# Performance work log

Measured on AMD Instinct MI355X. Metric: run time of the kernel, lower is better.

The kernel has to match this reference:

```python
import jax, jax.numpy as jnp
import numpy as np

B, LR_DIM, G_DIM, K, D, T = 256, 1024, 512, 64, 256, 8
GRID = jnp.linspace(-4.0, 4.0, 41)  # registered buffer in torch module


def _mu_bell(x, c, a_bell, b_bell):
    # generalized bell membership, clamp(a,b) >= 1e-3 as in torch
    a = jnp.maximum(a_bell, 1e-3)
    b = jnp.maximum(b_bell, 1e-3)
    return 1.0 / (1.0 + jnp.abs((x - c) / a) ** (2.0 * b))


def _mu_s(x, a, b):
    eps = 1e-12
    a2 = jnp.minimum(a, b)
    b2 = jnp.maximum(a, b)
    mid = (a2 + b2) * 0.5
    up = 2.0 * ((x - a2) / (b2 - a2 + eps)) ** 2
    dn = 1.0 - 2.0 * ((b2 - x) / (b2 - a2 + eps)) ** 2
    y = jnp.where((x > a2) & (x <= mid), up, jnp.zeros_like(x))
    y = jnp.where((x > mid) & (x <= b2), dn, y)
    return jnp.where(x > b2, jnp.ones_like(x), y)


def _fuzzify(x, a_bell, b_bell):
    # x: (B,d) -> (B,2d)
    xs = 4.0 * jnp.tanh(x / 4.0)
    xb = _mu_bell(xs, 0.0, a_bell, b_bell)
    xS = _mu_s(xs, -1.0, 1.0)
    return jnp.concatenate([xb, xS], axis=-1)


def _defuzzify(rt, a_bell, b_bell):
    # rt: (B,2d) -> centroid (B,d)
    d = rt.shape[1] // 2
    rb, rs = rt[:, :d], rt[:, d:]
    g = GRID[None, None, :]                      # (1,1,G)
    c_b = 4.0 * jnp.tanh(rb)[..., None]          # (B,d,1)
    c_s = 4.0 * jnp.tanh(rs)[..., None]
    mu_b = _mu_bell(g, c_b, a_bell, b_bell)      # (B,d,G)
    a_s = jnp.clip(c_s - 1.0, -4.0, 4.0)
    b_s = jnp.clip(c_s + 1.0, -4.0, 4.0)
    mu_s = _mu_s(g, a_s, b_s)
    cen_b = (g * mu_b).sum(-1) / (mu_b.sum(-1) + 1e-12)
    cen_s = (g * mu_s).sum(-1) / (mu_s.sum(-1) + 1e-12)
    return 0.5 * cen_b + 0.5 * cen_s


def _forward(wsi_lr, genomics, FT, W_lr, b_lr, W_g, b_g, WqI, WqG, WkI, WkG,
             WvI, WvG, mlp_W1, mlp_b1, mlp_W2, mlp_b2, Wf, bf, Wi, bi, Vf, Vi,
             a_bell, b_bell):
    scale = jnp.float32(D) ** 0.5
    lr = wsi_lr @ W_lr + b_lr                    # (B,d)
    g = genomics @ W_g + b_g
    lr_f = _fuzzify(lr, a_bell, b_bell)          # (B,2d)
    g_f = _fuzzify(g, a_bell, b_bell)
    QI = lr_f @ WqI                              # (B,d), loop-invariant
    QG = g_f @ WqG
    Ft0 = jnp.broadcast_to(FT[None], (wsi_lr.shape[0],) + FT.shape)  # (B,K,d)

    def step(Ft, _):
        sI = jnp.einsum('bd,bkd->bk', QI, Ft @ WkI) / scale
        sG = jnp.einsum('bd,bkd->bk', QG, Ft @ WkG) / scale
        rtI = jnp.einsum('bk,bke->be', jax.nn.softmax(sI, axis=-1), Ft @ WvI)  # (B,2d)
        rtG = jnp.einsum('bk,bke->be', jax.nn.softmax(sG, axis=-1), Ft @ WvG)
        r = 0.5 * _defuzzify(rtI, a_bell, b_bell) + 0.5 * _defuzzify(rtG, a_bell, b_bell)
        rb = jnp.broadcast_to(r[:, None, :], Ft.shape)              # (B,K,d)
        x = Ft + rb
        F_tilde = jax.nn.gelu(x @ mlp_W1 + mlp_b1, approximate=False) @ mlp_W2 + mlp_b2 + x
        f_gate = jax.nn.sigmoid(rb @ Wf + bf + jnp.tanh(Ft @ Vf))
        i_gate = jax.nn.sigmoid(rb @ Wi + bi + jnp.tanh(Ft @ Vi))
        Ft_new = f_gate * Ft + i_gate * jnp.tanh(F_tilde)
        return Ft_new, Ft_new

    _, steps = jax.lax.scan(step, Ft0, None, length=T)
    # torch stores step `T-s` result at index s-1: list index 0 holds the LAST
    # computed state, index T-1 the first -> reverse chronological order
    return steps[::-1]  # (T,B,K,d)


def setup_inputs() -> dict:
    key = jax.random.key(0)
    ks = jax.random.split(key, 20)

    def rn(k, shape, scale):
        return jax.random.normal(k, shape, dtype=jnp.float32) * scale

    z = lambda *s: jnp.zeros(s, jnp.float32)
    return dict(
        wsi_lr=rn(ks[0], (B, LR_DIM), 1.0),
        genomics=rn(ks[1], (B, G_DIM), 1.0),
        FT=rn(ks[2], (K, D), 0.02),
        W_lr=rn(ks[3], (LR_DIM, D), LR_DIM ** -0.5), b_lr=z(D),
        W_g=rn(ks[4], (G_DIM, D), G_DIM ** -0.5), b_g=z(D),
        WqI=rn(ks[5], (2 * D, D), (2 * D) ** -0.5),
        WqG=rn(ks[6], (2 * D, D), (2 * D) ** -0.5),
        WkI=rn(ks[7], (D, D), D ** -0.5),
        WkG=rn(ks[8], (D, D), D ** -0.5),
        WvI=rn(ks[9], (D, 2 * D), D ** -0.5),
        WvG=rn(ks[10], (D, 2 * D), D ** -0.5),
        mlp_W1=rn(ks[11], (D, 2 * D), D ** -0.5), mlp_b1=z(2 * D),
        mlp_W2=rn(ks[12], (2 * D, D), (2 * D) ** -0.5), mlp_b2=z(D),
        Wf=rn(ks[13], (D, D), D ** -0.5), bf=z(D),
        Wi=rn(ks[14], (D, D), D ** -0.5), bi=z(D),
        Vf=rn(ks[15], (D, D), D ** -0.5),
        Vi=rn(ks[16], (D, D), D ** -0.5),
        a_bell=jnp.float32(1.0),
        b_bell=jnp.float32(2.0),
    )


def reference(wsi_lr, genomics, FT, W_lr, b_lr, W_g, b_g, WqI, WqG, WkI, WkG,
              WvI, WvG, mlp_W1, mlp_b1, mlp_W2, mlp_b2, Wf, bf, Wi, bi, Vf, Vi,
              a_bell, b_bell):
    return _forward(wsi_lr, genomics, FT, W_lr, b_lr, W_g, b_g, WqI, WqG, WkI,
                    WkG, WvI, WvG, mlp_W1, mlp_b1, mlp_W2, mlp_b2, Wf, bf, Wi,
                    bi, Vf, Vi, a_bell, b_bell)
```

## Files before the change

kernel.cpp:

```cpp
#include <hip/hip_runtime.h>
#include <hip/hip_bf16.h>

#define B_    256
#define K_    64
#define D_    256
#define T_    8
#define NROW  (B_*K_)

typedef short short8v __attribute__((ext_vector_type(8)));
typedef float f32x4  __attribute__((ext_vector_type(4)));

__device__ __forceinline__ float fexp2(float x) { return __builtin_amdgcn_exp2f(x); }
__device__ __forceinline__ float flog2(float x) { return __builtin_amdgcn_logf(x); }

__device__ __forceinline__ float sigmoid_f(float x) {
  return 1.f / (1.f + fexp2(x * -1.4426950408889634f));
}
__device__ __forceinline__ float tanh_fast(float x) {
  float xc = fminf(fmaxf(x, -30.f), 30.f);
  float t = fexp2(xc * 2.8853900817779268f);
  return (t - 1.f) / (t + 1.f);
}
__device__ __forceinline__ float gelu_f(float x) {
  return 0.5f * x * (1.f + erff(x * 0.70710678118654752440f));
}
__device__ __forceinline__ unsigned short f2bf(float x) {
  __hip_bfloat16 h = __float2bfloat16(x);
  return *reinterpret_cast<unsigned short*>(&h);
}
__device__ __forceinline__ float bfss(unsigned short s) {
  return __uint_as_float(((unsigned int)s) << 16);
}
__device__ __forceinline__ float muS_f(float x, float a2, float b2) {
  float mid = 0.5f * (a2 + b2);
  float inv = 1.f / (b2 - a2 + 1e-12f);
  if (x > b2)  return 1.f;
  if (x > mid) { float u = (b2 - x) * inv; return 1.f - 2.f * u * u; }
  if (x > a2)  { float u = (x - a2) * inv; return 2.f * u * u; }
  return 0.f;
}
__device__ __forceinline__ float pow_abs(float z, float e2b) {
  return fexp2(e2b * flog2(fabsf(z)));
}
__device__ __forceinline__ float defuzz_one(float rb_, float rs_, float ab, float bb) {
  float e2b = 2.f * bb;
  float inv_ab = 1.f / ab;
  float cb = 4.f * tanh_fast(rb_);
  float num = 0.f, den = 0.f;
  #pragma unroll
  for (int j = 0; j < 41; ++j) {
    float gj = -4.f + 0.2f * (float)j;
    float mu = 1.f / (1.f + pow_abs((gj - cb) * inv_ab, e2b));
    num += gj * mu; den += mu;
  }
  float cenb = num / (den + 1e-12f);
  float cs = 4.f * tanh_fast(rs_);
  float as_ = fminf(fmaxf(cs - 1.f, -4.f), 4.f);
  float bs_ = fminf(fmaxf(cs + 1.f, -4.f), 4.f);
  num = 0.f; den = 0.f;
  {
    float mid = 0.5f * (as_ + bs_);
    float inv = 1.f / (bs_ - as_ + 1e-12f);
    #pragma unroll
    for (int j = 0; j < 41; ++j) {
      float gj = -4.f + 0.2f * (float)j;
      float mu;
      if (gj > bs_)      mu = 1.f;
      else if (gj > mid) { float u = (bs_ - gj) * inv; mu = 1.f - 2.f * u * u; }
      else if (gj > as_) { float u = (gj - as_) * inv; mu = 2.f * u * u; }
      else               mu = 0.f;
      num += gj * mu; den += mu;
    }
  }
  float cens = num / (den + 1e-12f);
  return 0.5f * cenb + 0.5f * cens;
}

__global__ __launch_bounds__(256) void k_convert(
    const float* __restrict__ W1, const float* __restrict__ Vf, const float* __restrict__ Vi,
    const float* __restrict__ W2, const float* __restrict__ FT,
    const float* __restrict__ WkI, const float* __restrict__ WkG,
    unsigned short* __restrict__ B1t, unsigned short* __restrict__ W2t,
    unsigned short* __restrict__ FTbf,
    float* __restrict__ WkIt, float* __restrict__ WkGt)
{
  int idx = blockIdx.x * 256 + threadIdx.x;
  if (idx < 262144) {
    int n = idx >> 8, k = idx & 255;
    float v = (n < 512) ? W1[(size_t)k*512 + n]
            : (n < 768) ? Vf[(size_t)k*256 + (n-512)]
                        : Vi[(size_t)k*256 + (n-768)];
    B1t[idx] = f2bf(v);
  } else if (idx < 393216) {
    int j = idx - 262144;
    int n = j >> 9, k = j & 511;
    W2t[j] = f2bf(W2[(size_t)k*256 + n]);
  } else if (idx < 409600) {
    int j = idx - 393216;
    FTbf[j] = f2bf(FT[j]);
  } else if (idx < 475136) {
    int j = idx - 409600;
    int k = j >> 8, n = j & 255;
    WkIt[j] = WkI[(size_t)n*256 + k];
  } else if (idx < 540672) {
    int j = idx - 475136;
    int k = j >> 8, n = j & 255;
    WkGt[j] = WkG[(size_t)n*256 + k];
  }
}

__global__ __launch_bounds__(256) void k_pre_lin(
    const float* __restrict__ wsi, const float* __restrict__ gen,
    const float* __restrict__ W_lr, const float* __restrict__ b_lr,
    const float* __restrict__ W_g,  const float* __restrict__ b_g,
    const float* __restrict__ a_p,  const float* __restrict__ b_p,
    float* __restrict__ lrf, float* __restrict__ gf)
{
  int g_ix = blockIdx.x;
  int half = g_ix >> 4, tile = g_ix & 15;
  int bx = tile & 3, by = tile >> 2;
  int n0 = bx * 64, m0 = by * 64;
  const float* A    = half ? gen  : wsi;
  const float* Bm   = half ? W_g  : W_lr;
  const float* bias = half ? b_g  : b_lr;
  float* outp       = half ? gf   : lrf;
  int KK            = half ? 512  : 1024;
  float ab = fmaxf(a_p[0], 0.001f), bb = fmaxf(b_p[0], 0.001f);
  float e2b = 2.f * bb, inv_ab = 1.f / ab;

  __shared__ float As[16][64];
  __shared__ float Bs[16][64];
  int tid = threadIdx.x, tx = tid & 15, ty = tid >> 4;
  float acc[4][4] = {};
  int am = tid >> 2, ak = (tid & 3) * 4;
  int bk = tid >> 4, bn = (tid & 15) * 4;
  const float* arow = A + (size_t)(m0 + am) * KK;
  for (int k0 = 0; k0 < KK; k0 += 16) {
    float4 av = *(const float4*)(arow + k0 + ak);
    As[ak+0][am] = av.x; As[ak+1][am] = av.y; As[ak+2][am] = av.z; As[ak+3][am] = av.w;
    *(float4*)&Bs[bk][bn] = *(const float4*)(Bm + (size_t)(k0 + bk) * 256 + n0 + bn);
    __syncthreads();
    #pragma unroll
    for (int kk = 0; kk < 16; ++kk) {
      float a0 = As[kk][ty*4+0], a1 = As[kk][ty*4+1], a2 = As[kk][ty*4+2], a3 = As[kk][ty*4+3];
      float b0 = Bs[kk][tx*4+0], b1 = Bs[kk][tx*4+1], b2 = Bs[kk][tx*4+2], b3 = Bs[kk][tx*4+3];
      acc[0][0]=fmaf(a0,b0,acc[0][0]); acc[0][1]=fmaf(a0,b1,acc[0][1]); acc[0][2]=fmaf(a0,b2,acc[0][2]); acc[0][3]=fmaf(a0,b3,acc[0][3]);
      acc[1][0]=fmaf(a1,b0,acc[1][0]); acc[1][1]=fmaf(a1,b1,acc[1][1]); acc[1][2]=fmaf(a1,b2,acc[1][2]); acc[1][3]=fmaf(a1,b3,acc[1][3]);
      acc[2][0]=fmaf(a2,b0,acc[2][0]); acc[2][1]=fmaf(a2,b1,acc[2][1]); acc[2][2]=fmaf(a2,b2,acc[2][2]); acc[2][3]=fmaf(a2,b3,acc[2][3]);
      acc[3][0]=fmaf(a3,b0,acc[3][0]); acc[3][1]=fmaf(a3,b1,acc[3][1]); acc[3][2]=fmaf(a3,b2,acc[3][2]); acc[3][3]=fmaf(a3,b3,acc[3][3]);
    }
    __syncthreads();
  }
  #pragma unroll
  for (int i = 0; i < 4; ++i) {
    int row = m0 + ty*4 + i;
    #pragma unroll
    for (int j = 0; j < 4; ++j) {
      int col = n0 + tx*4 + j;
      float v = acc[i][j] + bias[col];
      float xs = 4.f * tanh_fast(v * 0.25f);
      outp[(size_t)row*512 + col]       = 1.f / (1.f + pow_abs(xs * inv_ab, e2b));
      outp[(size_t)row*512 + col + 256] = muS_f(xs, -1.f, 1.f);
    }
  }
}

__global__ __launch_bounds__(256) void k_pre_q(
    const float* __restrict__ lrf, const float* __restrict__ gf,
    const float* __restrict__ WqI, const float* __restrict__ WqG,
    float* __restrict__ QI, float* __restrict__ QG)
{
  int g_ix = blockIdx.x;
  int half = g_ix >> 4, tile = g_ix & 15;
  int bx = tile & 3, by = tile >> 2;
  int n0 = bx * 64, m0 = by * 64;
  const float* A  = half ? gf  : lrf;
  const float* Bm = half ? WqG : WqI;
  float* outp     = half ? QG  : QI;

  __shared__ float As[16][64];
  __shared__ float Bs[16][64];
  int tid = threadIdx.x, tx = tid & 15, ty = tid >> 4;
  float acc[4][4] = {};
  int am = tid >> 2, ak = (tid & 3) * 4;
  int bk = tid >> 4, bn = (tid & 15) * 4;
  const float* arow = A + (size_t)(m0 + am) * 512;
  for (int k0 = 0; k0 < 512; k0 += 16) {
    float4 av = *(const float4*)(arow + k0 + ak);
    As[ak+0][am] = av.x; As[ak+1][am] = av.y; As[ak+2][am] = av.z; As[ak+3][am] = av.w;
    *(float4*)&Bs[bk][bn] = *(const float4*)(Bm + (size_t)(k0 + bk) * 256 + n0 + bn);
    __syncthreads();
    #pragma unroll
    for (int kk = 0; kk < 16; ++kk) {
      float a0 = As[kk][ty*4+0], a1 = As[kk][ty*4+1], a2 = As[kk][ty*4+2], a3 = As[kk][ty*4+3];
      float b0 = Bs[kk][tx*4+0], b1 = Bs[kk][tx*4+1], b2 = Bs[kk][tx*4+2], b3 = Bs[kk][tx*4+3];
      acc[0][0]=fmaf(a0,b0,acc[0][0]); acc[0][1]=fmaf(a0,b1,acc[0][1]); acc[0][2]=fmaf(a0,b2,acc[0][2]); acc[0][3]=fmaf(a0,b3,acc[0][3]);
      acc[1][0]=fmaf(a1,b0,acc[1][0]); acc[1][1]=fmaf(a1,b1,acc[1][1]); acc[1][2]=fmaf(a1,b2,acc[1][2]); acc[1][3]=fmaf(a1,b3,acc[1][3]);
      acc[2][0]=fmaf(a2,b0,acc[2][0]); acc[2][1]=fmaf(a2,b1,acc[2][1]); acc[2][2]=fmaf(a2,b2,acc[2][2]); acc[2][3]=fmaf(a2,b3,acc[2][3]);
      acc[3][0]=fmaf(a3,b0,acc[3][0]); acc[3][1]=fmaf(a3,b1,acc[3][1]); acc[3][2]=fmaf(a3,b2,acc[3][2]); acc[3][3]=fmaf(a3,b3,acc[3][3]);
    }
    __syncthreads();
  }
  #pragma unroll
  for (int i = 0; i < 4; ++i) {
    float4 v = make_float4(acc[i][0], acc[i][1], acc[i][2], acc[i][3]);
    *(float4*)(outp + (size_t)(m0 + ty*4 + i) * 256 + n0 + tx*4) = v;
  }
}

__global__ __launch_bounds__(256) void k_pre_qp(
    const float* __restrict__ QI, const float* __restrict__ QG,
    const float* __restrict__ WkIt, const float* __restrict__ WkGt,
    float* __restrict__ qIp, float* __restrict__ qGp)
{
  int g_ix = blockIdx.x;
  int half = g_ix >> 4, tile = g_ix & 15;
  int bx = tile & 3, by = tile >> 2;
  int n0 = bx * 64, m0 = by * 64;
  const float* A  = half ? QG   : QI;
  const float* Bm = half ? WkGt : WkIt;
  float* outp     = half ? qGp  : qIp;

  __shared__ float As[16][64];
  __shared__ float Bs[16][64];
  int tid = threadIdx.x, tx = tid & 15, ty = tid >> 4;
  float acc[4][4] = {};
  int am = tid >> 2, ak = (tid & 3) * 4;
  int bk = tid >> 4, bn = (tid & 15) * 4;
  const float* arow = A + (size_t)(m0 + am) * 256;
  for (int k0 = 0; k0 < 256; k0 += 16) {
    float4 av = *(const float4*)(arow + k0 + ak);
    As[ak+0][am] = av.x; As[ak+1][am] = av.y; As[ak+2][am] = av.z; As[ak+3][am] = av.w;
    *(float4*)&Bs[bk][bn] = *(const float4*)(Bm + (size_t)(k0 + bk) * 256 + n0 + bn);
    __syncthreads();
    #pragma unroll
    for (int kk = 0; kk < 16; ++kk) {
      float a0 = As[kk][ty*4+0], a1 = As[kk][ty*4+1], a2 = As[kk][ty*4+2], a3 = As[kk][ty*4+3];
      float b0 = Bs[kk][tx*4+0], b1 = Bs[kk][tx*4+1], b2 = Bs[kk][tx*4+2], b3 = Bs[kk][tx*4+3];
      acc[0][0]=fmaf(a0,b0,acc[0][0]); acc[0][1]=fmaf(a0,b1,acc[0][1]); acc[0][2]=fmaf(a0,b2,acc[0][2]); acc[0][3]=fmaf(a0,b3,acc[0][3]);
      acc[1][0]=fmaf(a1,b0,acc[1][0]); acc[1][1]=fmaf(a1,b1,acc[1][1]); acc[1][2]=fmaf(a1,b2,acc[1][2]); acc[1][3]=fmaf(a1,b3,acc[1][3]);
      acc[2][0]=fmaf(a2,b0,acc[2][0]); acc[2][1]=fmaf(a2,b1,acc[2][1]); acc[2][2]=fmaf(a2,b2,acc[2][2]); acc[2][3]=fmaf(a2,b3,acc[2][3]);
      acc[3][0]=fmaf(a3,b0,acc[3][0]); acc[3][1]=fmaf(a3,b1,acc[3][1]); acc[3][2]=fmaf(a3,b2,acc[3][2]); acc[3][3]=fmaf(a3,b3,acc[3][3]);
    }
    __syncthreads();
  }
  #pragma unroll
  for (int i = 0; i < 4; ++i) {
    float4 v = make_float4(acc[i][0], acc[i][1], acc[i][2], acc[i][3]);
    *(float4*)(outp + (size_t)(m0 + ty*4 + i) * 256 + n0 + tx*4) = v;
  }
}

__global__ __launch_bounds__(256) void k_ftbar(
    const unsigned short* __restrict__ Fb_all, int bcast,
    const float* __restrict__ qIp, const float* __restrict__ qGp,
    float* __restrict__ ftbI, float* __restrict__ ftbG)
{
  __shared__ __align__(16) char smem[38912];
  int b = blockIdx.x, t = threadIdx.x;
  short* Fs  = (short*)smem;
  float* qv  = (float*)(smem + 33792);
  float* red = (float*)(smem + 35840);
  float* prl = (float*)(smem + 37888);

  const unsigned short* Fsrc = bcast ? Fb_all : (Fb_all + (size_t)b * K_ * D_);
  #pragma unroll
  for (int i = 0; i < 8; ++i) {
    int sidx = (i * 256 + t) * 8;
    int row = sidx >> 8, col = sidx & 255;
    *(float4*)&Fs[row * 264 + col] = *(const float4*)&Fsrc[sidx];
  }
  qv[t]       = qIp[(size_t)b*256 + t];
  qv[256 + t] = qGp[(size_t)b*256 + t];
  __syncthreads();
  {
    int k = t & 63, part = t >> 6;
    const unsigned int* frow = (const unsigned int*)&Fs[k * 264 + part * 64];
    const float* q0 = qv + part * 64;
    const float* q1 = qv + 256 + part * 64;
    float s0 = 0.f, s1 = 0.f;
    #pragma unroll
    for (int d2 = 0; d2 < 32; ++d2) {
      unsigned int pr = frow[d2];
      float f0 = __uint_as_float(pr << 16);
      float f1 = __uint_as_float(pr & 0xffff0000u);
      s0 = fmaf(f1, q0[2*d2+1], fmaf(f0, q0[2*d2], s0));
      s1 = fmaf(f1, q1[2*d2+1], fmaf(f0, q1[2*d2], s1));
    }
    red[t] = s0; red[256 + t] = s1;
  }
  __syncthreads();
  if (t < 128) {
    int which = t >> 6, kk = t & 63;
    const float* rp = red + which * 256;
    float s = (rp[kk] + rp[64+kk] + rp[128+kk] + rp[192+kk]) * (1.f/16.f);
    float m = s;
    for (int off = 32; off; off >>= 1) m = fmaxf(m, __shfl_xor(m, off, 64));
    float e = fexp2((s - m) * 1.4426950408889634f);
    float sum = e;
    for (int off = 32; off; off >>= 1) sum += __shfl_xor(sum, off, 64);
    prl[which * 64 + kk] = e / sum;
  }
  __syncthreads();
  {
    float f0 = 0.f, f1 = 0.f;
    #pragma unroll 8
    for (int kk = 0; kk < 64; ++kk) {
      float fv = bfss((unsigned short)Fs[kk * 264 + t]);
      f0 = fmaf(prl[kk],      fv, f0);
      f1 = fmaf(prl[64 + kk], fv, f1);
    }
    ftbI[(size_t)b*256 + t] = f0;
    ftbG[(size_t)b*256 + t] = f1;
  }
}

__global__ __launch_bounds__(256) void k_rt(
    const float* __restrict__ ftbI, const float* __restrict__ ftbG,
    const float* __restrict__ WvI,  const float* __restrict__ WvG,
    float* __restrict__ rt)
{
  int bx = blockIdx.x & 15, by = blockIdx.x >> 4;
  int n0 = bx * 64, m0 = by * 64;
  const float* Ap = (n0 < 512) ? ftbI : ftbG;
  const float* Bp = (n0 < 512) ? WvI  : WvG;
  int nb = (n0 < 512) ? n0 : n0 - 512;
  __shared__ float As[16][64];
  __shared__ float Bs[16][64];
  int tid = threadIdx.x, tx = tid & 15, ty = tid >> 4;
  float acc[4][4] = {};
  int am = tid >> 2, ak = (tid & 3) * 4;
  int bk = tid >> 4, bn = (tid & 15) * 4;
  const float* arow = Ap + (size_t)(m0 + am) * 256;
  for (int k0 = 0; k0 < 256; k0 += 16) {
    float4 av = *(const float4*)(arow + k0 + ak);
    As[ak+0][am] = av.x; As[ak+1][am] = av.y; As[ak+2][am] = av.z; As[ak+3][am] = av.w;
    *(float4*)&Bs[bk][bn] = *(const float4*)(Bp + (size_t)(k0 + bk) * 512 + nb + bn);
    __syncthreads();
    #pragma unroll
    for (int kk = 0; kk < 16; ++kk) {
      float a0 = As[kk][ty*4+0], a1 = As[kk][ty*4+1], a2 = As[kk][ty*4+2], a3 = As[kk][ty*4+3];
      float b0 = Bs[kk][tx*4+0], b1 = Bs[kk][tx*4+1], b2 = Bs[kk][tx*4+2], b3 = Bs[kk][tx*4+3];
      acc[0][0]=fmaf(a0,b0,acc[0][0]); acc[0][1]=fmaf(a0,b1,acc[0][1]); acc[0][2]=fmaf(a0,b2,acc[0][2]); acc[0][3]=fmaf(a0,b3,acc[0][3]);
      acc[1][0]=fmaf(a1,b0,acc[1][0]); acc[1][1]=fmaf(a1,b1,acc[1][1]); acc[1][2]=fmaf(a1,b2,acc[1][2]); acc[1][3]=fmaf(a1,b3,acc[1][3]);
      acc[2][0]=fmaf(a2,b0,acc[2][0]); acc[2][1]=fmaf(a2,b1,acc[2][1]); acc[2][2]=fmaf(a2,b2,acc[2][2]); acc[2][3]=fmaf(a2,b3,acc[2][3]);
      acc[3][0]=fmaf(a3,b0,acc[3][0]); acc[3][1]=fmaf(a3,b1,acc[3][1]); acc[3][2]=fmaf(a3,b2,acc[3][2]); acc[3][3]=fmaf(a3,b3,acc[3][3]);
    }
    __syncthreads();
  }
  #pragma unroll
  for (int i = 0; i < 4; ++i) {
    float4 v = make_float4(acc[i][0], acc[i][1], acc[i][2], acc[i][3]);
    *(float4*)(rt + (size_t)(m0 + ty*4 + i) * 1024 + n0 + tx*4) = v;
  }
}

__global__ __launch_bounds__(256) void k_defuzz(
    const float* __restrict__ rt,
    const float* __restrict__ a_p, const float* __restrict__ b_p,
    float* __restrict__ r_out)
{
  int b = blockIdx.x, t = threadIdx.x;
  float ab = fmaxf(a_p[0], 0.001f), bb = fmaxf(b_p[0], 0.001f);
  const float* rb = rt + (size_t)b * 1024;
  float rI = defuzz_one(rb[t],       rb[256 + t], ab, bb);
  float rG = defuzz_one(rb[512 + t], rb[768 + t], ab, bb);
  r_out[(size_t)b*256 + t] = 0.5f * rI + 0.5f * rG;
}

__global__ __launch_bounds__(256) void k_rW(
    const float* __restrict__ r,
    const float* __restrict__ W1, const float* __restrict__ Wf, const float* __restrict__ Wi,
    float* __restrict__ rW1, float* __restrict__ rWf, float* __restrict__ rWi)
{
  int bx = blockIdx.x & 15, by = blockIdx.x >> 4;
  int n0 = bx * 64, m0 = by * 64;
  const float* Bp; int ldb, nb;
  if (n0 < 512)      { Bp = W1; ldb = 512; nb = n0; }
  else if (n0 < 768) { Bp = Wf; ldb = 256; nb = n0 - 512; }
  else               { Bp = Wi; ldb = 256; nb = n0 - 768; }
  __shared__ float As[16][64];
  __shared__ float Bs[16][64];
  int tid = threadIdx.x, tx = tid & 15, ty = tid >> 4;
  float acc[4][4] = {};
  int am = tid >> 2, ak = (tid & 3) * 4;
  int bk = tid >> 4, bn = (tid & 15) * 4;
  const float* arow = r + (size_t)(m0 + am) * 256;
  for (int k0 = 0; k0 < 256; k0 += 16) {
    float4 av = *(const float4*)(arow + k0 + ak);
    As[ak+0][am] = av.x; As[ak+1][am] = av.y; As[ak+2][am] = av.z; As[ak+3][am] = av.w;
    *(float4*)&Bs[bk][bn] = *(const float4*)(Bp + (size_t)(k0 + bk) * ldb + nb + bn);
    __syncthreads();
    #pragma unroll
    for (int kk = 0; kk < 16; ++kk) {
      float a0 = As[kk][ty*4+0], a1 = As[kk][ty*4+1], a2 = As[kk][ty*4+2], a3 = As[kk][ty*4+3];
      float b0 = Bs[kk][tx*4+0], b1 = Bs[kk][tx*4+1], b2 = Bs[kk][tx*4+2], b3 = Bs[kk][tx*4+3];
      acc[0][0]=fmaf(a0,b0,acc[0][0]); acc[0][1]=fmaf(a0,b1,acc[0][1]); acc[0][2]=fmaf(a0,b2,acc[0][2]); acc[0][3]=fmaf(a0,b3,acc[0][3]);
      acc[1][0]=fmaf(a1,b0,acc[1][0]); acc[1][1]=fmaf(a1,b1,acc[1][1]); acc[1][2]=fmaf(a1,b2,acc[1][2]); acc[1][3]=fmaf(a1,b3,acc[1][3]);
      acc[2][0]=fmaf(a2,b0,acc[2][0]); acc[2][1]=fmaf(a2,b1,acc[2][1]); acc[2][2]=fmaf(a2,b2,acc[2][2]); acc[2][3]=fmaf(a2,b3,acc[2][3]);
      acc[3][0]=fmaf(a3,b0,acc[3][0]); acc[3][1]=fmaf(a3,b1,acc[3][1]); acc[3][2]=fmaf(a3,b2,acc[3][2]); acc[3][3]=fmaf(a3,b3,acc[3][3]);
    }
    __syncthreads();
  }
  #pragma unroll
  for (int i = 0; i < 4; ++i) {
    int row = m0 + ty*4 + i;
    float4 v = make_float4(acc[i][0], acc[i][1], acc[i][2], acc[i][3]);
    int c = tx * 4;
    if (n0 < 512)      *(float4*)(rW1 + (size_t)row*512 + n0 + c)        = v;
    else if (n0 < 768) *(float4*)(rWf + (size_t)row*256 + (n0-512) + c)  = v;
    else               *(float4*)(rWi + (size_t)row*256 + (n0-768) + c)  = v;
  }
}

__global__ __launch_bounds__(512) void k_g1(
    const unsigned short* __restrict__ Fb_all, int bcast,
    const unsigned short* __restrict__ B1t,
    const float* __restrict__ rW1, const float* __restrict__ b1,
    const float* __restrict__ rWf, const float* __restrict__ bfv,
    const float* __restrict__ rWi, const float* __restrict__ biv,
    unsigned short* __restrict__ A2, unsigned short* __restrict__ Gf, unsigned short* __restrict__ Gi)
{
  __shared__ __align__(16) short Fs[64*264];
  __shared__ __align__(16) short Bst[2][64*264];
  int b = blockIdx.x, tid = threadIdx.x;
  int w = tid >> 6, lane = tid & 63, lr = lane & 15, lh = lane >> 4;
  int wm = w >> 2, wn = w & 3;

  const unsigned short* Fsrc = bcast ? Fb_all : (Fb_all + (size_t)b * 64 * 256);
  #pragma unroll
  for (int p = 0; p < 8; ++p) {
    int idx = (p*512 + tid) * 8;
    int row = idx >> 8, col = idx & 255;
    *(float4*)&Fs[row*264 + col] = *(const float4*)&Fsrc[idx];
  }
  #pragma unroll
  for (int p = 0; p < 8; ++p) {
    int idx = (p*512 + tid) * 8;
    int row = idx >> 8, col = idx & 255;
    *(float4*)&Bst[0][row*264 + col] = *(const float4*)&B1t[idx];
  }
  __syncthreads();

  short8v afr0[8], afr1[8];
  #pragma unroll
  for (int ks = 0; ks < 8; ++ks) {
    afr0[ks] = *(const short8v*)&Fs[(wm*32 + lr)*264      + ks*32 + lh*8];
    afr1[ks] = *(const short8v*)&Fs[(wm*32 + 16 + lr)*264 + ks*32 + lh*8];
  }

  for (int c = 0; c < 16; ++c) {
    float4 pf[8];
    if (c < 15) {
      const unsigned short* src = B1t + (size_t)(c+1) * 64 * 256;
      #pragma unroll
      for (int p = 0; p < 8; ++p) pf[p] = *(const float4*)&src[(p*512 + tid)*8];
    }
    f32x4 acc0 = {0.f,0.f,0.f,0.f}, acc1 = {0.f,0.f,0.f,0.f};
    const short* Bb = Bst[c & 1];
    #pragma unroll
    for (int ks = 0; ks < 8; ++ks) {
      short8v bf_ = *(const short8v*)&Bb[(wn*16 + lr)*264 + ks*32 + lh*8];
      acc0 = __builtin_amdgcn_mfma_f32_16x16x32_bf16(afr0[ks], bf_, acc0, 0, 0, 0);
      acc1 = __builtin_amdgcn_mfma_f32_16x16x32_bf16(afr1[ks], bf_, acc1, 0, 0, 0);
    }
    int col = c*64 + wn*16 + lr;
    if (col < 512) {
      float add = rW1[(size_t)b*512 + col] + b1[col];
      #pragma unroll
      for (int r = 0; r < 4; ++r) {
        int row0 = b*64 + wm*32 + lh*4 + r;
        A2[(size_t)row0*512 + col]      = f2bf(gelu_f(acc0[r] + add));
        A2[(size_t)(row0+16)*512 + col] = f2bf(gelu_f(acc1[r] + add));
      }
    } else if (col < 768) {
      int cc = col - 512;
      float add = rWf[(size_t)b*256 + cc] + bfv[cc];
      #pragma unroll
      for (int r = 0; r < 4; ++r) {
        int row0 = b*64 + wm*32 + lh*4 + r;
        Gf[(size_t)row0*256 + cc]      = f2bf(sigmoid_f(add + tanh_fast(acc0[r])));
        Gf[(size_t)(row0+16)*256 + cc] = f2bf(sigmoid_f(add + tanh_fast(acc1[r])));
      }
    } else {
      int cc = col - 768;
      float add = rWi[(size_t)b*256 + cc] + biv[cc];
      #pragma unroll
      for (int r = 0; r < 4; ++r) {
        int row0 = b*64 + wm*32 + lh*4 + r;
        Gi[(size_t)row0*256 + cc]      = f2bf(sigmoid_f(add + tanh_fast(acc0[r])));
        Gi[(size_t)(row0+16)*256 + cc] = f2bf(sigmoid_f(add + tanh_fast(acc1[r])));
      }
    }
    if (c < 15) {
      short* Bn = Bst[(c+1) & 1];
      #pragma unroll
      for (int p = 0; p < 8; ++p) {
        int idx = (p*512 + tid) * 8;
        int row = idx >> 8, colk = idx & 255;
        *(float4*)&Bn[row*264 + colk] = pf[p];
      }
      __syncthreads();
    }
  }
}

__global__ __launch_bounds__(512) void k_g2(
    const unsigned short* __restrict__ A2, const unsigned short* __restrict__ W2t,
    const float* __restrict__ b2,
    const float* __restrict__ Fprev, const float* __restrict__ FT, int bcast,
    const float* __restrict__ rr,
    const unsigned short* __restrict__ Gf, const unsigned short* __restrict__ Gi,
    float* __restrict__ Fout, unsigned short* __restrict__ Fbf)
{
  __shared__ __align__(16) short As2[64*520];
  __shared__ __align__(16) short Wst[2][32*520];
  int b = blockIdx.x, tid = threadIdx.x;
  int w = tid >> 6, lane = tid & 63, lr = lane & 15, lh = lane >> 4;
  int wm = w >> 1, wn = w & 1;

  const unsigned short* Asrc = A2 + (size_t)b * 64 * 512;
  #pragma unroll
  for (int p = 0; p < 8; ++p) {
    int idx = (p*512 + tid) * 8;
    int row = idx >> 9, col = idx & 511;
    *(float4*)&As2[row*520 + col] = *(const float4*)&Asrc[idx];
  }
  #pragma unroll
  for (int p = 0; p < 4; ++p) {
    int idx = (p*512 + tid) * 8;
    int row = idx >> 9, col = idx & 511;
    *(float4*)&Wst[0][row*520 + col] = *(const float4*)&W2t[idx];
  }
  __syncthreads();

  short8v afr[16];
  #pragma unroll
  for (int ks = 0; ks < 16; ++ks)
    afr[ks] = *(const short8v*)&As2[(wm*16 + lr)*520 + ks*32 + lh*8];

  for (int c = 0; c < 8; ++c) {
    float4 pf[4];
    if (c < 7) {
      const unsigned short* src = W2t + (size_t)(c+1) * 32 * 512;
      #pragma unroll
      for (int p = 0; p < 4; ++p) pf[p] = *(const float4*)&src[(p*512 + tid)*8];
    }
    f32x4 acc = {0.f,0.f,0.f,0.f};
    const short* Wb = Wst[c & 1];
    #pragma unroll
    for (int ks = 0; ks < 16; ++ks) {
      short8v bf_ = *(const short8v*)&Wb[(wn*16 + lr)*520 + ks*32 + lh*8];
      acc = __builtin_amdgcn_mfma_f32_16x16x32_bf16(afr[ks], bf_, acc, 0, 0, 0);
    }
    int col = c*32 + wn*16 + lr;
    float b2c = b2[col], rv = rr[(size_t)b*256 + col];
    #pragma unroll
    for (int r = 0; r < 4; ++r) {
      int row = b*64 + wm*16 + lh*4 + r;
      float Ftv = bcast ? FT[(size_t)(row & 63)*256 + col]
                        : Fprev[(size_t)row*256 + col];
      float ftld = acc[r] + b2c + Ftv + rv;
      float fg = bfss(Gf[(size_t)row*256 + col]);
      float ig = bfss(Gi[(size_t)row*256 + col]);
      float ov = fg * Ftv + ig * tanh_fast(ftld);
      Fout[(size_t)row*256 + col] = ov;
      Fbf[(size_t)row*256 + col] = f2bf(ov);
    }
    if (c < 7) {
      short* Wn = Wst[(c+1) & 1];
      #pragma unroll
      for (int p = 0; p < 4; ++p) {
        int idx = (p*512 + tid) * 8;
        int row = idx >> 9, colk = idx & 511;
        *(float4*)&Wn[row*520 + colk] = pf[p];
      }
      __syncthreads();
    }
  }
}

extern "C" void kernel_launch(void* const* d_in, const int* in_sizes, int n_in,
                              void* d_out, int out_size, void* d_ws, size_t ws_size,
                              hipStream_t stream)
{
  (void)in_sizes; (void)n_in; (void)out_size; (void)ws_size;
  const float* wsi  = (const float*)d_in[0];
  const float* gen  = (const float*)d_in[1];
  const float* FT   = (const float*)d_in[2];
  const float* W_lr = (const float*)d_in[3];
  const float* b_lr = (const float*)d_in[4];
  const float* W_g  = (const float*)d_in[5];
  const float* b_g  = (const float*)d_in[6];
  const float* WqI  = (const float*)d_in[7];
  const float* WqG  = (const float*)d_in[8];
  const float* WkI  = (const float*)d_in[9];
  const float* WkG  = (const float*)d_in[10];
  const float* WvI  = (const float*)d_in[11];
  const float* WvG  = (const float*)d_in[12];
  const float* W1   = (const float*)d_in[13];
  const float* b1   = (const float*)d_in[14];
  const float* W2   = (const float*)d_in[15];
  const float* b2   = (const float*)d_in[16];
  const float* Wf   = (const float*)d_in[17];
  const float* bf   = (const float*)d_in[18];
  const float* Wi   = (const float*)d_in[19];
  const float* bi   = (const float*)d_in[20];
  const float* Vf   = (const float*)d_in[21];
  const float* Vi   = (const float*)d_in[22];
  const float* a_p  = (const float*)d_in[23];
  const float* b_p  = (const float*)d_in[24];

  float* out = (float*)d_out;
  float* ws  = (float*)d_ws;
  float* rr    = ws;
  float* rW1   = rr    + 65536;
  float* rWf   = rW1   + 131072;
  float* rWi   = rWf   + 65536;
  float* qIp   = rWi   + 65536;
  float* qGp   = qIp   + 65536;
  float* lrf   = qGp   + 65536;
  float* gf    = lrf   + 131072;
  float* QI    = gf    + 131072;
  float* QG    = QI    + 65536;
  float* WkIt  = QG    + 65536;
  float* WkGt  = WkIt  + 65536;
  float* ftbI  = WkGt  + 65536;
  float* ftbG  = ftbI  + 65536;
  float* rt    = ftbG  + 65536;
  unsigned short* A2   = (unsigned short*)(rt + 262144);
  unsigned short* Gfb  = A2   + 8388608;
  unsigned short* Gib  = Gfb  + 4194304;
  unsigned short* Fbf  = Gib  + 4194304;
  unsigned short* FTbf = Fbf  + 4194304;
  unsigned short* B1t  = FTbf + 16384;
  unsigned short* W2t  = B1t  + 262144;

  k_convert<<<2112, 256, 0, stream>>>(W1, Vf, Vi, W2, FT, WkI, WkG,
                                      B1t, W2t, FTbf, WkIt, WkGt);
  k_pre_lin<<<32, 256, 0, stream>>>(wsi, gen, W_lr, b_lr, W_g, b_g, a_p, b_p, lrf, gf);
  k_pre_q<<<32, 256, 0, stream>>>(lrf, gf, WqI, WqG, QI, QG);
  k_pre_qp<<<32, 256, 0, stream>>>(QI, QG, WkIt, WkGt, qIp, qGp);

  const float* Fcur = nullptr;
  int bcast = 1;
  for (int st = 0; st < T_; ++st) {
    float* Fnext = out + (size_t)(7 - st) * NROW * D_;
    k_ftbar<<<256, 256, 0, stream>>>(bcast ? FTbf : Fbf, bcast, qIp, qGp, ftbI, ftbG);
    k_rt<<<64, 256, 0, stream>>>(ftbI, ftbG, WvI, WvG, rt);
    k_defuzz<<<256, 256, 0, stream>>>(rt, a_p, b_p, rr);
    k_rW<<<64, 256, 0, stream>>>(rr, W1, Wf, Wi, rW1, rWf, rWi);
    k_g1<<<256, 512, 0, stream>>>(bcast ? FTbf : Fbf, bcast, B1t,
                                  rW1, b1, rWf, bf, rWi, bi, A2, Gfb, Gib);
    k_g2<<<256, 512, 0, stream>>>(A2, W2t, b2, Fcur, FT, bcast, rr,
                                  Gfb, Gib, Fnext, Fbf);
    Fcur = Fnext;
    bcast = 0;
  }
}
```

Measured before the change: 972.3 us.

## Fuse the two MLP GEMM kernels into one, keeping activations in LDS

Merges k_g1 and k_g2 into a single per-batch kernel. The GELU hidden activations (A2) stay in shared memory instead of going to global memory, and the forget/input gates are packed as bf16 pairs in registers and consumed directly by the second GEMM's epilogue. This removes the global write and read of A2, Gf and Gi, plus one launch per step. In exchange shared-memory use per block grows and register pressure rises, and the W2 tiles are no longer double-buffered.

```diff
diff --git a/kernel.cpp b/kernel.cpp
--- a/kernel.cpp
+++ b/kernel.cpp
@@ -413,51 +413,52 @@
   }
 }
 
-__global__ __launch_bounds__(512) void k_g1(
+__global__ __launch_bounds__(512) void k_mega(
     const unsigned short* __restrict__ Fb_all, int bcast,
     const unsigned short* __restrict__ B1t,
+    const unsigned short* __restrict__ W2t,
     const float* __restrict__ rW1, const float* __restrict__ b1,
     const float* __restrict__ rWf, const float* __restrict__ bfv,
     const float* __restrict__ rWi, const float* __restrict__ biv,
-    unsigned short* __restrict__ A2, unsigned short* __restrict__ Gf, unsigned short* __restrict__ Gi)
-{
-  __shared__ __align__(16) short Fs[64*264];
-  __shared__ __align__(16) short Bst[2][64*264];
+    const float* __restrict__ b2,  const float* __restrict__ rr,
+    const float* __restrict__ Fprev, const float* __restrict__ FT,
+    float* __restrict__ Fout, unsigned short* __restrict__ Fbf)
+{
+  __shared__ __align__(16) short A2ls[64*520];
+  __shared__ __align__(16) short Sbuf[2*64*264];
   int b = blockIdx.x, tid = threadIdx.x;
   int w = tid >> 6, lane = tid & 63, lr = lane & 15, lh = lane >> 4;
   int wm = w >> 2, wn = w & 3;
 
   const unsigned short* Fsrc = bcast ? Fb_all : (Fb_all + (size_t)b * 64 * 256);
   #pragma unroll
-  for (int p = 0; p < 8; ++p) {
+  for (int p = 0; p < 4; ++p) {
     int idx = (p*512 + tid) * 8;
     int row = idx >> 8, col = idx & 255;
-    *(float4*)&Fs[row*264 + col] = *(const float4*)&Fsrc[idx];
-  }
-  #pragma unroll
-  for (int p = 0; p < 8; ++p) {
-    int idx = (p*512 + tid) * 8;
-    int row = idx >> 8, col = idx & 255;
-    *(float4*)&Bst[0][row*264 + col] = *(const float4*)&B1t[idx];
+    *(float4*)&A2ls[row*264 + col] = *(const float4*)&Fsrc[idx];
+    *(float4*)&Sbuf[row*264 + col] = *(const float4*)&B1t[idx];
   }
   __syncthreads();
-
   short8v afr0[8], afr1[8];
   #pragma unroll
   for (int ks = 0; ks < 8; ++ks) {
-    afr0[ks] = *(const short8v*)&Fs[(wm*32 + lr)*264      + ks*32 + lh*8];
-    afr1[ks] = *(const short8v*)&Fs[(wm*32 + 16 + lr)*264 + ks*32 + lh*8];
-  }
-
+    afr0[ks] = *(const short8v*)&A2ls[(wm*32 + lr)*264      + ks*32 + lh*8];
+    afr1[ks] = *(const short8v*)&A2ls[(wm*32 + 16 + lr)*264 + ks*32 + lh*8];
+  }
+  __syncthreads();
+
+  unsigned int fgp[4][4], igp[4][4];
+
+  #pragma unroll
   for (int c = 0; c < 16; ++c) {
-    float4 pf[8];
+    float4 pf[4];
     if (c < 15) {
       const unsigned short* src = B1t + (size_t)(c+1) * 64 * 256;
       #pragma unroll
-      for (int p = 0; p < 8; ++p) pf[p] = *(const float4*)&src[(p*512 + tid)*8];
+      for (int p = 0; p < 4; ++p) pf[p] = *(const float4*)&src[(p*512 + tid)*8];
     }
     f32x4 acc0 = {0.f,0.f,0.f,0.f}, acc1 = {0.f,0.f,0.f,0.f};
-    const short* Bb = Bst[c & 1];
+    const short* Bb = &Sbuf[(c & 1) * 16896];
     #pragma unroll
     for (int ks = 0; ks < 8; ++ks) {
       short8v bf_ = *(const short8v*)&Bb[(wn*16 + lr)*264 + ks*32 + lh*8];
@@ -465,118 +466,82 @@
       acc1 = __builtin_amdgcn_mfma_f32_16x16x32_bf16(afr1[ks], bf_, acc1, 0, 0, 0);
     }
     int col = c*64 + wn*16 + lr;
-    if (col < 512) {
+    if (c < 8) {
       float add = rW1[(size_t)b*512 + col] + b1[col];
       #pragma unroll
       for (int r = 0; r < 4; ++r) {
-        int row0 = b*64 + wm*32 + lh*4 + r;
-        A2[(size_t)row0*512 + col]      = f2bf(gelu_f(acc0[r] + add));
-        A2[(size_t)(row0+16)*512 + col] = f2bf(gelu_f(acc1[r] + add));
+        int row0 = wm*32 + lh*4 + r;
+        A2ls[row0*520 + col]      = f2bf(gelu_f(acc0[r] + add));
+        A2ls[(row0+16)*520 + col] = f2bf(gelu_f(acc1[r] + add));
       }
-    } else if (col < 768) {
+    } else if (c < 12) {
       int cc = col - 512;
       float add = rWf[(size_t)b*256 + cc] + bfv[cc];
       #pragma unroll
-      for (int r = 0; r < 4; ++r) {
-        int row0 = b*64 + wm*32 + lh*4 + r;
-        Gf[(size_t)row0*256 + cc]      = f2bf(sigmoid_f(add + tanh_fast(acc0[r])));
-        Gf[(size_t)(row0+16)*256 + cc] = f2bf(sigmoid_f(add + tanh_fast(acc1[r])));
-      }
+      for (int r = 0; r < 4; ++r)
+        fgp[c-8][r] = (((unsigned int)f2bf(sigmoid_f(add + tanh_fast(acc1[r])))) << 16)
+                    |  (unsigned int)f2bf(sigmoid_f(add + tanh_fast(acc0[r])));
     } else {
       int cc = col - 768;
       float add = rWi[(size_t)b*256 + cc] + biv[cc];
       #pragma unroll
-      for (int r = 0; r < 4; ++r) {
-        int row0 = b*64 + wm*32 + lh*4 + r;
-        Gi[(size_t)row0*256 + cc]      = f2bf(sigmoid_f(add + tanh_fast(acc0[r])));
-        Gi[(size_t)(row0+16)*256 + cc] = f2bf(sigmoid_f(add + tanh_fast(acc1[r])));
-      }
+      for (int r = 0; r < 4; ++r)
+        igp[c-12][r] = (((unsigned int)f2bf(sigmoid_f(add + tanh_fast(acc1[r])))) << 16)
+                     |  (unsigned int)f2bf(sigmoid_f(add + tanh_fast(acc0[r])));
     }
     if (c < 15) {
-      short* Bn = Bst[(c+1) & 1];
+      short* Bn = &Sbuf[((c+1) & 1) * 16896];
       #pragma unroll
-      for (int p = 0; p < 8; ++p) {
+      for (int p = 0; p < 4; ++p) {
         int idx = (p*512 + tid) * 8;
         int row = idx >> 8, colk = idx & 255;
         *(float4*)&Bn[row*264 + colk] = pf[p];
       }
-      __syncthreads();
-    }
-  }
-}
-
-__global__ __launch_bounds__(512) void k_g2(
-    const unsigned short* __restrict__ A2, const unsigned short* __restrict__ W2t,
-    const float* __restrict__ b2,
-    const float* __restrict__ Fprev, const float* __restrict__ FT, int bcast,
-    const float* __restrict__ rr,
-    const unsigned short* __restrict__ Gf, const unsigned short* __restrict__ Gi,
-    float* __restrict__ Fout, unsigned short* __restrict__ Fbf)
-{
-  __shared__ __align__(16) short As2[64*520];
-  __shared__ __align__(16) short Wst[2][32*520];
-  int b = blockIdx.x, tid = threadIdx.x;
-  int w = tid >> 6, lane = tid & 63, lr = lane & 15, lh = lane >> 4;
-  int wm = w >> 1, wn = w & 1;
-
-  const unsigned short* Asrc = A2 + (size_t)b * 64 * 512;
-  #pragma unroll
-  for (int p = 0; p < 8; ++p) {
-    int idx = (p*512 + tid) * 8;
-    int row = idx >> 9, col = idx & 511;
-    *(float4*)&As2[row*520 + col] = *(const float4*)&Asrc[idx];
-  }
-  #pragma unroll
-  for (int p = 0; p < 4; ++p) {
-    int idx = (p*512 + tid) * 8;
-    int row = idx >> 9, col = idx & 511;
-    *(float4*)&Wst[0][row*520 + col] = *(const float4*)&W2t[idx];
-  }
-  __syncthreads();
-
-  short8v afr[16];
-  #pragma unroll
-  for (int ks = 0; ks < 16; ++ks)
-    afr[ks] = *(const short8v*)&As2[(wm*16 + lr)*520 + ks*32 + lh*8];
-
-  for (int c = 0; c < 8; ++c) {
-    float4 pf[4];
-    if (c < 7) {
-      const unsigned short* src = W2t + (size_t)(c+1) * 32 * 512;
-      #pragma unroll
-      for (int p = 0; p < 4; ++p) pf[p] = *(const float4*)&src[(p*512 + tid)*8];
-    }
-    f32x4 acc = {0.f,0.f,0.f,0.f};
-    const short* Wb = Wst[c & 1];
+    }
+    __syncthreads();
+  }
+
+  #pragma unroll
+  for (int k = 0; k < 4; ++k) {
+    const unsigned short* wsrc = W2t + (size_t)k * 64 * 512;
+    #pragma unroll
+    for (int p = 0; p < 8; ++p) {
+      int idx = (p*512 + tid) * 8;
+      int row = idx >> 9, colk = idx & 511;
+      *(float4*)&Sbuf[row*520 + colk] = *(const float4*)&wsrc[idx];
+    }
+    __syncthreads();
+    f32x4 o0 = {0.f,0.f,0.f,0.f}, o1 = {0.f,0.f,0.f,0.f};
     #pragma unroll
     for (int ks = 0; ks < 16; ++ks) {
-      short8v bf_ = *(const short8v*)&Wb[(wn*16 + lr)*520 + ks*32 + lh*8];
-      acc = __builtin_amdgcn_mfma_f32_16x16x32_bf16(afr[ks], bf_, acc, 0, 0, 0);
-    }
-    int col = c*32 + wn*16 + lr;
+      short8v a0 = *(const short8v*)&A2ls[(wm*32 + lr)*520      + ks*32 + lh*8];
+      short8v a1 = *(const short8v*)&A2ls[(wm*32 + 16 + lr)*520 + ks*32 + lh*8];
+      short8v bw = *(const short8v*)&Sbuf[(wn*16 + lr)*520      + ks*32 + lh*8];
+      o0 = __builtin_amdgcn_mfma_f32_16x16x32_bf16(a0, bw, o0, 0, 0, 0);
+      o1 = __builtin_amdgcn_mfma_f32_16x16x32_bf16(a1, bw, o1, 0, 0, 0);
+    }
+    int col = k*64 + wn*16 + lr;
     float b2c = b2[col], rv = rr[(size_t)b*256 + col];
     #pragma unroll
     for (int r = 0; r < 4; ++r) {
-      int row = b*64 + wm*16 + lh*4 + r;
-      float Ftv = bcast ? FT[(size_t)(row & 63)*256 + col]
-                        : Fprev[(size_t)row*256 + col];
-      float ftld = acc[r] + b2c + Ftv + rv;
-      float fg = bfss(Gf[(size_t)row*256 + col]);
-      float ig = bfss(Gi[(size_t)row*256 + col]);
+      int row = b*64 + wm*32 + lh*4 + r;
+      float Ftv = bcast ? FT[(size_t)(row & 63)*256 + col] : Fprev[(size_t)row*256 + col];
+      float fg = bfss((unsigned short)(fgp[k][r] & 0xffffu));
+      float ig = bfss((unsigned short)(igp[k][r] & 0xffffu));
+      float ftld = o0[r] + b2c + Ftv + rv;
       float ov = fg * Ftv + ig * tanh_fast(ftld);
       Fout[(size_t)row*256 + col] = ov;
       Fbf[(size_t)row*256 + col] = f2bf(ov);
-    }
-    if (c < 7) {
-      short* Wn = Wst[(c+1) & 1];
-      #pragma unroll
-      for (int p = 0; p < 4; ++p) {
-        int idx = (p*512 + tid) * 8;
-        int row = idx >> 9, colk = idx & 511;
-        *(float4*)&Wn[row*520 + colk] = pf[p];
-      }
-      __syncthreads();
-    }
+      int row2 = row + 16;
+      float Ftv2 = bcast ? FT[(size_t)(row2 & 63)*256 + col] : Fprev[(size_t)row2*256 + col];
+      float fg2 = bfss((unsigned short)(fgp[k][r] >> 16));
+      float ig2 = bfss((unsigned short)(igp[k][r] >> 16));
+      float ftld2 = o1[r] + b2c + Ftv2 + rv;
+      float ov2 = fg2 * Ftv2 + ig2 * tanh_fast(ftld2);
+      Fout[(size_t)row2*256 + col] = ov2;
+      Fbf[(size_t)row2*256 + col] = f2bf(ov2);
+    }
+    if (k < 3) __syncthreads();
   }
 }
 
@@ -628,10 +593,7 @@
   float* ftbI  = WkGt  + 65536;
   float* ftbG  = ftbI  + 65536;
   float* rt    = ftbG  + 65536;
-  unsigned short* A2   = (unsigned short*)(rt + 262144);
-  unsigned short* Gfb  = A2   + 8388608;
-  unsigned short* Gib  = Gfb  + 4194304;
-  unsigned short* Fbf  = Gib  + 4194304;
+  unsigned short* Fbf  = (unsigned short*)(rt + 262144);
   unsigned short* FTbf = Fbf  + 4194304;
   unsigned short* B1t  = FTbf + 16384;
   unsigned short* W2t  = B1t  + 262144;
@@ -650,10 +612,9 @@
     k_rt<<<64, 256, 0, stream>>>(ftbI, ftbG, WvI, WvG, rt);
     k_defuzz<<<256, 256, 0, stream>>>(rt, a_p, b_p, rr);
     k_rW<<<64, 256, 0, stream>>>(rr, W1, Wf, Wi, rW1, rWf, rWi);
-    k_g1<<<256, 512, 0, stream>>>(bcast ? FTbf : Fbf, bcast, B1t,
-                                  rW1, b1, rWf, bf, rWi, bi, A2, Gfb, Gib);
-    k_g2<<<256, 512, 0, stream>>>(A2, W2t, b2, Fcur, FT, bcast, rr,
-                                  Gfb, Gib, Fnext, Fbf);
+    k_mega<<<256, 512, 0, stream>>>(bcast ? FTbf : Fbf, bcast, B1t, W2t,
+                                    rW1, b1, rWf, bf, rWi, bi, b2, rr,
+                                    Fcur, FT, Fnext, Fbf);
     Fcur = Fnext;
     bcast = 0;
   }
```

Measured after the change: 1.494 ms. 53.6% more time.

## Fuse attention-pooling ftbar into k_g2 epilogue and load MFMA A fragments from global

Applied to the files above, without the earlier changes.

The per-step attention pooling (softmax over K and weighted sum of F) now runs at the end of k_g2, using the bf16 F tile that block just wrote, so the separate k_ftbar launch is kept only for step 0. This removes seven kernel launches and one re-read pass over F per run. k_g1 and k_g2 also load their A-operand fragments straight from global memory into registers instead of staging them through LDS, which frees shared memory. The B1t prefetch in k_g1 is cut to the 64-row chunk it actually uses; the old loop loaded twice that. The fused tail adds LDS reuse and extra barriers in k_g2, and it relies on each block reading back its own global writes after __syncthreads.

```diff
diff --git a/kernel.cpp b/kernel.cpp
--- a/kernel.cpp
+++ b/kernel.cpp
@@ -421,40 +421,32 @@
     const float* __restrict__ rWi, const float* __restrict__ biv,
     unsigned short* __restrict__ A2, unsigned short* __restrict__ Gf, unsigned short* __restrict__ Gi)
 {
-  __shared__ __align__(16) short Fs[64*264];
   __shared__ __align__(16) short Bst[2][64*264];
   int b = blockIdx.x, tid = threadIdx.x;
   int w = tid >> 6, lane = tid & 63, lr = lane & 15, lh = lane >> 4;
   int wm = w >> 2, wn = w & 3;
 
   const unsigned short* Fsrc = bcast ? Fb_all : (Fb_all + (size_t)b * 64 * 256);
-  #pragma unroll
-  for (int p = 0; p < 8; ++p) {
-    int idx = (p*512 + tid) * 8;
-    int row = idx >> 8, col = idx & 255;
-    *(float4*)&Fs[row*264 + col] = *(const float4*)&Fsrc[idx];
-  }
-  #pragma unroll
-  for (int p = 0; p < 8; ++p) {
+  short8v afr0[8], afr1[8];
+  #pragma unroll
+  for (int ks = 0; ks < 8; ++ks) {
+    afr0[ks] = *(const short8v*)&Fsrc[(size_t)(wm*32 + lr)*256      + ks*32 + lh*8];
+    afr1[ks] = *(const short8v*)&Fsrc[(size_t)(wm*32 + 16 + lr)*256 + ks*32 + lh*8];
+  }
+  #pragma unroll
+  for (int p = 0; p < 4; ++p) {
     int idx = (p*512 + tid) * 8;
     int row = idx >> 8, col = idx & 255;
     *(float4*)&Bst[0][row*264 + col] = *(const float4*)&B1t[idx];
   }
   __syncthreads();
 
-  short8v afr0[8], afr1[8];
-  #pragma unroll
-  for (int ks = 0; ks < 8; ++ks) {
-    afr0[ks] = *(const short8v*)&Fs[(wm*32 + lr)*264      + ks*32 + lh*8];
-    afr1[ks] = *(const short8v*)&Fs[(wm*32 + 16 + lr)*264 + ks*32 + lh*8];
-  }
-
   for (int c = 0; c < 16; ++c) {
-    float4 pf[8];
+    float4 pf[4];
     if (c < 15) {
-      const unsigned short* src = B1t + (size_t)(c+1) * 64 * 256;
+      const unsigned short* src = B1t + (size_t)(c+1) * 16384;
       #pragma unroll
-      for (int p = 0; p < 8; ++p) pf[p] = *(const float4*)&src[(p*512 + tid)*8];
+      for (int p = 0; p < 4; ++p) pf[p] = *(const float4*)&src[(p*512 + tid)*8];
     }
     f32x4 acc0 = {0.f,0.f,0.f,0.f}, acc1 = {0.f,0.f,0.f,0.f};
     const short* Bb = Bst[c & 1];
@@ -495,7 +487,7 @@
     if (c < 15) {
       short* Bn = Bst[(c+1) & 1];
       #pragma unroll
-      for (int p = 0; p < 8; ++p) {
+      for (int p = 0; p < 4; ++p) {
         int idx = (p*512 + tid) * 8;
         int row = idx >> 8, colk = idx & 255;
         *(float4*)&Bn[row*264 + colk] = pf[p];
@@ -511,21 +503,21 @@
     const float* __restrict__ Fprev, const float* __restrict__ FT, int bcast,
     const float* __restrict__ rr,
     const unsigned short* __restrict__ Gf, const unsigned short* __restrict__ Gi,
-    float* __restrict__ Fout, unsigned short* __restrict__ Fbf)
-{
-  __shared__ __align__(16) short As2[64*520];
-  __shared__ __align__(16) short Wst[2][32*520];
+    float* __restrict__ Fout, unsigned short* __restrict__ Fbf,
+    const float* __restrict__ qIp, const float* __restrict__ qGp,
+    float* __restrict__ ftbI, float* __restrict__ ftbG, int do_ftbar)
+{
+  __shared__ __align__(16) char smem[66560];
+  short (*Wst)[32*520] = (short (*)[32*520])smem;
   int b = blockIdx.x, tid = threadIdx.x;
   int w = tid >> 6, lane = tid & 63, lr = lane & 15, lh = lane >> 4;
   int wm = w >> 1, wn = w & 1;
 
-  const unsigned short* Asrc = A2 + (size_t)b * 64 * 512;
-  #pragma unroll
-  for (int p = 0; p < 8; ++p) {
-    int idx = (p*512 + tid) * 8;
-    int row = idx >> 9, col = idx & 511;
-    *(float4*)&As2[row*520 + col] = *(const float4*)&Asrc[idx];
-  }
+  short8v afr[16];
+  #pragma unroll
+  for (int ks = 0; ks < 16; ++ks)
+    afr[ks] = *(const short8v*)&A2[(size_t)(b*64 + wm*16 + lr)*512 + ks*32 + lh*8];
+
   #pragma unroll
   for (int p = 0; p < 4; ++p) {
     int idx = (p*512 + tid) * 8;
@@ -534,15 +526,10 @@
   }
   __syncthreads();
 
-  short8v afr[16];
-  #pragma unroll
-  for (int ks = 0; ks < 16; ++ks)
-    afr[ks] = *(const short8v*)&As2[(wm*16 + lr)*520 + ks*32 + lh*8];
-
   for (int c = 0; c < 8; ++c) {
     float4 pf[4];
     if (c < 7) {
-      const unsigned short* src = W2t + (size_t)(c+1) * 32 * 512;
+      const unsigned short* src = W2t + (size_t)(c+1) * 16384;
       #pragma unroll
       for (int p = 0; p < 4; ++p) pf[p] = *(const float4*)&src[(p*512 + tid)*8];
     }
@@ -550,8 +537,8 @@
     const short* Wb = Wst[c & 1];
     #pragma unroll
     for (int ks = 0; ks < 16; ++ks) {
-      short8v bf_ = *(const short8v*)&Wb[(wn*16 + lr)*520 + ks*32 + lh*8];
-      acc = __builtin_amdgcn_mfma_f32_16x16x32_bf16(afr[ks], bf_, acc, 0, 0, 0);
+      short8v bw = *(const short8v*)&Wb[(wn*16 + lr)*520 + ks*32 + lh*8];
+      acc = __builtin_amdgcn_mfma_f32_16x16x32_bf16(afr[ks], bw, acc, 0, 0, 0);
     }
     int col = c*32 + wn*16 + lr;
     float b2c = b2[col], rv = rr[(size_t)b*256 + col];
@@ -577,6 +564,63 @@
       }
       __syncthreads();
     }
+  }
+
+  if (!do_ftbar) return;
+  __syncthreads();
+
+  short* Fs  = (short*)smem;
+  float* qv  = (float*)(smem + 33792);
+  float* red = (float*)(smem + 35840);
+  float* prl = (float*)(smem + 37888);
+  int t = tid;
+  const unsigned short* Fsrc = Fbf + (size_t)b * 64 * 256;
+  #pragma unroll
+  for (int i = 0; i < 4; ++i) {
+    int sidx = (i * 512 + t) * 8;
+    int row = sidx >> 8, col = sidx & 255;
+    *(float4*)&Fs[row * 264 + col] = *(const float4*)&Fsrc[sidx];
+  }
+  if (t < 256) qv[t] = qIp[(size_t)b*256 + t];
+  else         qv[t] = qGp[(size_t)b*256 + (t - 256)];
+  __syncthreads();
+  {
+    int which = t >> 8, tt = t & 255;
+    int k = tt & 63, part = tt >> 6;
+    const unsigned int* frow = (const unsigned int*)&Fs[k * 264 + part * 64];
+    const float* q0 = qv + which*256 + part * 64;
+    float s0 = 0.f;
+    #pragma unroll
+    for (int d2 = 0; d2 < 32; ++d2) {
+      unsigned int pr = frow[d2];
+      float f0 = __uint_as_float(pr << 16);
+      float f1 = __uint_as_float(pr & 0xffff0000u);
+      s0 = fmaf(f1, q0[2*d2+1], fmaf(f0, q0[2*d2], s0));
+    }
+    red[which*256 + tt] = s0;
+  }
+  __syncthreads();
+  if (t < 128) {
+    int which = t >> 6, kk = t & 63;
+    const float* rp = red + which * 256;
+    float s = (rp[kk] + rp[64+kk] + rp[128+kk] + rp[192+kk]) * (1.f/16.f);
+    float m = s;
+    for (int off = 32; off; off >>= 1) m = fmaxf(m, __shfl_xor(m, off, 64));
+    float e = fexp2((s - m) * 1.4426950408889634f);
+    float sum = e;
+    for (int off = 32; off; off >>= 1) sum += __shfl_xor(sum, off, 64);
+    prl[which * 64 + kk] = e / sum;
+  }
+  __syncthreads();
+  {
+    int which = t >> 8, tt = t & 255;
+    const float* pp = prl + which * 64;
+    float f0 = 0.f;
+    #pragma unroll 8
+    for (int kk = 0; kk < 64; ++kk)
+      f0 = fmaf(pp[kk], bfss((unsigned short)Fs[kk * 264 + tt]), f0);
+    if (which == 0) ftbI[(size_t)b*256 + tt] = f0;
+    else            ftbG[(size_t)b*256 + tt] = f0;
   }
 }
 
@@ -646,14 +690,16 @@
   int bcast = 1;
   for (int st = 0; st < T_; ++st) {
     float* Fnext = out + (size_t)(7 - st) * NROW * D_;
-    k_ftbar<<<256, 256, 0, stream>>>(bcast ? FTbf : Fbf, bcast, qIp, qGp, ftbI, ftbG);
+    if (st == 0)
+      k_ftbar<<<256, 256, 0, stream>>>(FTbf, 1, qIp, qGp, ftbI, ftbG);
     k_rt<<<64, 256, 0, stream>>>(ftbI, ftbG, WvI, WvG, rt);
     k_defuzz<<<256, 256, 0, stream>>>(rt, a_p, b_p, rr);
     k_rW<<<64, 256, 0, stream>>>(rr, W1, Wf, Wi, rW1, rWf, rWi);
     k_g1<<<256, 512, 0, stream>>>(bcast ? FTbf : Fbf, bcast, B1t,
                                   rW1, b1, rWf, bf, rWi, bi, A2, Gfb, Gib);
     k_g2<<<256, 512, 0, stream>>>(A2, W2t, b2, Fcur, FT, bcast, rr,
-                                  Gfb, Gib, Fnext, Fbf);
+                                  Gfb, Gib, Fnext, Fbf,
+                                  qIp, qGp, ftbI, ftbG, (st < 7) ? 1 : 0);
     Fcur = Fnext;
     bcast = 0;
   }
```

Result: slower. 1.065 ms (+9.5%).
